# Kernel optimization log

Hardware: AMD Instinct MI355X
Metric: run time of the kernel (lower is better)

## Reference

```python
import jax, jax.numpy as jnp
from jax import lax
import numpy as np

V, D, H, E, L, B = 512, 128, 64, 4, 60, 4096
ADJ = 184  # ((180 + 7) // 8) * 8


def setup_inputs() -> dict:
    key = jax.random.key(0)
    it = iter(jax.random.split(key, 64))

    def nrm(shape, s=0.05):
        return jax.random.normal(next(it), shape, dtype=jnp.float32) * s

    x = jax.random.randint(next(it), (B, L), 0, V, dtype=jnp.int32)
    inp = {"x": x, "emb": nrm((V, D), 0.02).at[0].set(0.0)}  # padding_idx=0 row zero
    for d in ("f", "r"):
        inp[f"w_ih_{d}"] = nrm((4 * H, D)); inp[f"w_hh_{d}"] = nrm((4 * H, H))
        inp[f"b_ih_{d}"] = nrm((4 * H,)); inp[f"b_hh_{d}"] = nrm((4 * H,))
    for p, i_, h_, o_ in (("e", 1, 16, 8), ("l", 1, 16, 8), ("c", V, 32, 16), ("p", 6, 24, 12), ("x", 4, 16, 8)):
        inp[f"{p}_w1"] = nrm((h_, i_)); inp[f"{p}_b1"] = nrm((h_,))
        inp[f"{p}_w2"] = nrm((o_, h_)); inp[f"{p}_b2"] = nrm((o_,))
    inp["fp_w"] = nrm((ADJ, 180)); inp["fp_b"] = nrm((ADJ,))
    inp["attn_w"] = nrm((3 * ADJ, ADJ)); inp["attn_b"] = nrm((3 * ADJ,))
    inp["out_w"] = nrm((ADJ, ADJ)); inp["out_b"] = nrm((ADJ,))
    for i, (o_, i_) in enumerate(((128, ADJ), (64, 128), (32, 64), (E, 32)), 1):
        inp[f"g_w{i}"] = nrm((o_, i_)); inp[f"g_b{i}"] = nrm((o_,))
    return inp


def _mlp2(h, w1, b1, w2, b2):
    return jnp.maximum(h @ w1.T + b1, 0.0) @ w2.T + b2


def _lstm_final(xe, w_ih, w_hh, b_ih, b_hh):
    # torch LSTM gate order i, f, g, o; returns final hidden state [B, H]
    xg = jnp.einsum('bld,gd->blg', xe, w_ih) + b_ih
    h0 = jnp.zeros((xe.shape[0], H), xe.dtype)

    def step(carry, g_t):
        h, c = carry
        g = g_t + h @ w_hh.T + b_hh
        i, f, gg, o = jnp.split(g, 4, axis=-1)
        c = jax.nn.sigmoid(f) * c + jax.nn.sigmoid(i) * jnp.tanh(gg)
        h = jax.nn.sigmoid(o) * jnp.tanh(c)
        return (h, c), None

    (h, _), _ = lax.scan(step, (h0, h0), jnp.swapaxes(xg, 0, 1))
    return h


def _sequence_stats(x):
    # Fully vectorized equivalent of the per-sequence python loops
    f32 = jnp.float32
    mask = x != 0
    vlen = mask.sum(1)                                       # [B]
    vlenf = jnp.maximum(vlen, 1).astype(f32)
    pos = jnp.arange(L)
    # per-row histogram over valid tokens (torch.bincount of valid_seq)
    counts = jnp.zeros((B, V), f32).at[jnp.arange(B)[:, None], x].add(mask.astype(f32))
    probs = counts / jnp.maximum(counts.sum(1, keepdims=True), 1.0)
    entropy = -jnp.sum(probs * jnp.log(probs + 1e-8), axis=1)
    entropy = jnp.where(vlen > 1, entropy, 0.0)
    char_dist = counts / vlenf[:, None]
    # compact valid tokens to the front (torch: seq[seq != 0]), stable argsort
    order = jnp.argsort((~mask).astype(jnp.int32), axis=1)
    cseq = jnp.take_along_axis(x, order, axis=1)
    cseq = jnp.where(pos[None] < vlen[:, None], cseq, 0)
    a, b = cseq[:, :-1], cseq[:, 1:]
    pairmask = pos[: L - 1][None] < (vlen - 1)[:, None]
    den1 = jnp.maximum(vlen - 1, 1).astype(f32)
    repeat = ((a == b) & pairmask).sum(1) / den1
    inc = ((b > a) & pairmask).sum(1) / den1
    dec = ((b < a) & pairmask).sum(1) / den1
    m2 = pos[: L - 2][None] < (vlen - 2)[:, None]
    per = ((cseq[:, :-2] == cseq[:, 2:]) & m2).sum(1) / jnp.maximum(vlen - 2, 1)
    per = jnp.where(vlen >= 4, per, 0.0)
    diversity = (counts > 0).sum(1) / vlenf
    # longest run of equal consecutive tokens via cummax of reset positions
    eq = jnp.concatenate([jnp.zeros((B, 1), bool), (cseq[:, 1:] == cseq[:, :-1]) & (pos[1:][None] < vlen[:, None])], 1)
    lastreset = lax.cummax(jnp.where(eq, -1, pos[None]), axis=1)
    runlen = pos[None] - lastreset + 1
    max_rep = jnp.where(pos[None] < vlen[:, None], runlen, 0).max(1) / vlenf
    pattern = jnp.stack([repeat, inc, dec, per, diversity, max_rep], 1).astype(f32)
    pattern = jnp.where((vlen > 1)[:, None], pattern, 0.0)
    # unique bigrams: sort pair codes, count distinct valid codes
    codes = jnp.where(pairmask, a * V + b, -1)
    s = jnp.sort(codes, axis=1)
    prevc = jnp.concatenate([jnp.full((B, 1), -2, s.dtype), s[:, :-1]], 1)
    comp_ratio = ((s != prevc) & (s >= 0)).sum(1) / den1
    info_density = entropy / jnp.log(jnp.maximum(vlen, 2).astype(f32))
    # local complexity: mean over sliding windows of (#unique / w), w = min(5, len//2)
    wsel = jnp.minimum(5, vlen // 2)
    local = jnp.zeros((B,), f32)
    for w in (2, 3, 4, 5):
        nwin = L - w + 1
        sh = [cseq[:, k:k + nwin] for k in range(w)]
        u = jnp.ones((B, nwin), f32)
        for k in range(1, w):
            isnew = jnp.ones((B, nwin), bool)
            for m in range(k):
                isnew = isnew & (sh[k] != sh[m])
            u = u + isnew
        winmask = pos[:nwin][None] < (vlen - w + 1)[:, None]
        lc = (u * winmask).sum(1) / w / jnp.maximum(vlen - w + 1, 1)
        local = jnp.where(wsel == w, lc, local)
    trans = 1.0 - repeat  # transitions/(len-1) == 1 - repeat_ratio
    complexity = jnp.stack([comp_ratio, info_density, local, trans], 1).astype(f32)
    complexity = jnp.where((vlen > 1)[:, None], complexity, 0.0)
    return entropy, vlen, char_dist, pattern, complexity


def reference(x, emb, w_ih_f, w_hh_f, b_ih_f, b_hh_f, w_ih_r, w_hh_r, b_ih_r, b_hh_r, e_w1, e_b1, e_w2, e_b2, l_w1, l_b1, l_w2, l_b2, c_w1, c_b1, c_w2, c_b2, p_w1, p_b1, p_w2, p_b2, x_w1, x_b1, x_w2, x_b2, fp_w, fp_b, attn_w, attn_b, out_w, out_b, g_w1, g_b1, g_w2, g_b2, g_w3, g_b3, g_w4, g_b4):
    entropy, vlen, char_dist, pattern, complexity = _sequence_stats(x)
    xe = emb[x]                                               # [B, L, D]
    h_f = _lstm_final(xe, w_ih_f, w_hh_f, b_ih_f, b_hh_f)
    h_r = _lstm_final(xe[:, ::-1], w_ih_r, w_hh_r, b_ih_r, b_hh_r)
    feats = jnp.concatenate([
        h_f, h_r,
        _mlp2((entropy / 4.0)[:, None], e_w1, e_b1, e_w2, e_b2),
        _mlp2((vlen.astype(jnp.float32) / 60.0)[:, None], l_w1, l_b1, l_w2, l_b2),
        _mlp2(char_dist, c_w1, c_b1, c_w2, c_b2),
        _mlp2(pattern, p_w1, p_b1, p_w2, p_b2),
        _mlp2(complexity, x_w1, x_b1, x_w2, x_b2),
    ], axis=1)                                                # [B, 180]
    f = feats @ fp_w.T + fp_b                                 # [B, 184]
    # MultiheadAttention with seq_len == 1: softmax over a single key is 1,
    # so attended = out_proj(v_proj(f)) exactly (q/k projections cancel).
    wv, bv = attn_w[2 * ADJ:], attn_b[2 * ADJ:]
    attended = (f @ wv.T + bv) @ out_w.T + out_b
    h = jnp.maximum(attended @ g_w1.T + g_b1, 0.0)
    h = jnp.maximum(h @ g_w2.T + g_b2, 0.0)
    h = jnp.maximum(h @ g_w3.T + g_b3, 0.0)
    logits = h @ g_w4.T + g_b4
    return jax.nn.softmax(logits, axis=-1)  # eval path (training=False)
```

## Files before the change

kernel.cpp:

```cpp
#include <hip/hip_runtime.h>

#define BATCH 4096
#define SEQL  60
#define VOC   512
#define EMBD  128
#define HID   64
#define GATES 256
#define ADJ   184

typedef __attribute__((ext_vector_type(8))) short short8;
typedef __attribute__((ext_vector_type(4))) float f32x4;

__device__ __forceinline__ float sigm(float x) {
  return __builtin_amdgcn_rcpf(1.f + __expf(-x));
}
__device__ __forceinline__ float tanh_(float x) {
  float e = __expf(2.f * x);
  return 1.f - 2.f * __builtin_amdgcn_rcpf(e + 1.f);
}
__device__ __forceinline__ unsigned short f2bf(float f) {
  unsigned int u = __float_as_uint(f);
  unsigned int r = (u + 0x7fffu + ((u >> 16) & 1u)) >> 16;
  return (unsigned short)r;
}
__device__ __forceinline__ float dot4(float4 a, float4 b, float acc) {
  acc = fmaf(a.x, b.x, acc); acc = fmaf(a.y, b.y, acc);
  acc = fmaf(a.z, b.z, acc); acc = fmaf(a.w, b.w, acc);
  return acc;
}
__device__ __forceinline__ float wsumf(float v) {
  #pragma unroll
  for (int s = 32; s > 0; s >>= 1) v += __shfl_xor(v, s, 64);
  return v;
}
__device__ __forceinline__ int wsumi(int v) {
  #pragma unroll
  for (int s = 32; s > 0; s >>= 1) v += __shfl_xor(v, s, 64);
  return v;
}
__device__ __forceinline__ int wmaxi(int v) {
  #pragma unroll
  for (int s = 32; s > 0; s >>= 1) v = max(v, __shfl_xor(v, s, 64));
  return v;
}

__global__ __launch_bounds__(256) void k_mega(
    const int* __restrict__ x, const float* __restrict__ emb,
    const float* __restrict__ wih_f, const float* __restrict__ bif, const float* __restrict__ bhf,
    const float* __restrict__ wih_r, const float* __restrict__ bir, const float* __restrict__ bhr,
    const float* __restrict__ whh_f, const float* __restrict__ whh_r,
    const float* __restrict__ g_w1, const float* __restrict__ g_b1,
    const float* __restrict__ out_w, const float* __restrict__ out_b,
    const float* __restrict__ attn_w, const float* __restrict__ attn_b,
    const float* __restrict__ fp_w, const float* __restrict__ fp_b,
    const float* __restrict__ g_w2, const float* __restrict__ g_w3,
    const float* __restrict__ g_w4, const float* __restrict__ c_w1,
    float* __restrict__ ent_o, float* __restrict__ vlen_o,
    float* __restrict__ pat_o, float* __restrict__ cpx_o,
    unsigned int* __restrict__ cnt_o,
    float* __restrict__ G_f, float* __restrict__ G_r,
    unsigned short* __restrict__ Wfrag,
    float* __restrict__ A, float* __restrict__ avb,
    float* __restrict__ Bp, float* __restrict__ vb,
    float* __restrict__ g_w2t, float* __restrict__ g_w3t, float* __restrict__ g_w4t,
    float* __restrict__ c_w1t) {
  __shared__ unsigned int cnt[4][512];
  __shared__ unsigned short q[4][68];
  const int bid = blockIdx.x;
  const int tid = threadIdx.x;

  if (bid < 1024) {
    const int lane = tid & 63;
    const int wid = tid >> 6;
    const int row = bid * 4 + wid;
    unsigned int* cr = cnt[wid];
    unsigned short* qr = q[wid];

    for (int i = lane; i < 512; i += 64) cr[i] = 0u;
    qr[lane] = 0;
    if (lane < 4) qr[64 + lane] = 0;
    int v = (lane < 60) ? x[row * 60 + lane] : 0;
    bool act = (v != 0);
    unsigned long long amask = __ballot(act);
    int n = __popcll(amask);
    __syncthreads();
    if (act) {
      int pos = __popcll(amask & ((1ull << lane) - 1ull));
      qr[pos] = (unsigned short)v;
      atomicAdd(&cr[v], 1u);
    }
    __syncthreads();

    float vlenf = (float)(n >= 1 ? n : 1);
    float inv = 1.f / vlenf;

    float ent = 0.f; int distinct = 0;
    #pragma unroll
    for (int j = 0; j < 8; j++) {
      unsigned int c = cr[lane + j * 64];
      if (c) {
        distinct++;
        float p = (float)c * inv;
        ent -= p * __logf(p + 1e-8f);
      }
    }
    ent = wsumf(ent);
    distinct = wsumi(distinct);

    int a = qr[lane], b = qr[lane + 1], c2 = qr[lane + 2];
    bool v1 = (lane + 1 < n);
    bool v2 = (lane + 2 < n);
    int rep  = __popcll(__ballot(v1 && (a == b)));
    int incs = __popcll(__ballot(v1 && (b > a)));
    int decs = __popcll(__ballot(v1 && (b < a)));
    int per2 = __popcll(__ballot(v2 && (a == c2)));

    int prev = (lane > 0) ? (int)qr[lane - 1] : -1;
    bool isst = (lane < n) && (lane == 0 || a != prev);
    unsigned long long smask = __ballot(isst);
    int len = 0;
    if (isst) {
      unsigned long long hi = (lane < 63) ? (smask >> (lane + 1)) : 0ull;
      int next = hi ? (lane + __ffsll((unsigned long long)hi)) : n;
      len = next - lane;
    }
    int maxrun = wmaxi(len);

    int code = v1 ? (a * VOC + b) : -1;
    int unique = v1 ? 1 : 0;
    #pragma unroll 1
    for (int j = 0; j < 58; j++) {
      int cj = __shfl(code, j, 64);
      if (j < lane && cj == code) unique = 0;
    }
    int dc = __popcll(__ballot(unique != 0));

    int wl = n >> 1; if (wl > 5) wl = 5;
    float local = 0.f;
    if (wl >= 2) {
      bool pv = (lane + wl <= n);
      int u = 0;
      if (pv) {
        int t0 = qr[lane], t1 = qr[lane + 1], t2 = qr[lane + 2];
        int t3 = qr[lane + 3], t4 = qr[lane + 4];
        u = 1;
        u += (t1 != t0);
        if (wl >= 3) u += (int)((t2 != t1) && (t2 != t0));
        if (wl >= 4) u += (int)((t3 != t2) && (t3 != t1) && (t3 != t0));
        if (wl >= 5) u += (int)((t4 != t3) && (t4 != t2) && (t4 != t1) && (t4 != t0));
      }
      int usum = wsumi(u);
      int denw = n - wl + 1; if (denw < 1) denw = 1;
      local = (float)usum / (float)wl / (float)denw;
    }

    float den1 = (float)((n - 1) >= 1 ? (n - 1) : 1);
    float repeat = (float)rep / den1;
    float per = (n >= 4) ? (float)per2 / (float)((n - 2) >= 1 ? (n - 2) : 1) : 0.f;
    float entz = (n > 1) ? ent : 0.f;
    float z = (n > 1) ? 1.f : 0.f;

    if (lane == 0) {
      ent_o[row] = entz;
      vlen_o[row] = (float)n;
      pat_o[row * 6 + 0] = repeat * z;
      pat_o[row * 6 + 1] = (float)incs / den1 * z;
      pat_o[row * 6 + 2] = (float)decs / den1 * z;
      pat_o[row * 6 + 3] = per * z;
      pat_o[row * 6 + 4] = (float)distinct * inv * z;
      pat_o[row * 6 + 5] = (float)maxrun * inv * z;
      cpx_o[row * 4 + 0] = (float)dc / den1 * z;
      cpx_o[row * 4 + 1] = entz / __logf((float)(n >= 2 ? n : 2)) * z;
      cpx_o[row * 4 + 2] = local * z;
      cpx_o[row * 4 + 3] = (1.f - repeat) * z;
    }
    for (int i = lane; i < 128; i += 64) {
      unsigned int p = cr[4 * i] | (cr[4 * i + 1] << 8) |
                       (cr[4 * i + 2] << 16) | (cr[4 * i + 3] << 24);
      cnt_o[row * 128 + i] = p;
    }
  } else if (bid < 1152) {
    const int bx = bid - 1024;
    const int dir = bx >> 6;
    const int rem = bx & 63;
    const int v0 = (rem >> 2) * 32;
    const int j0 = (rem & 3) * 64;
    const float* W = dir ? wih_r : wih_f;
    const float* bi = dir ? bir : bif;
    const float* bh = dir ? bhr : bhf;
    float* G = dir ? G_r : G_f;
    const int vp = tid >> 4;
    const int jq = tid & 15;
    const int v = v0 + vp * 2;
    const int j = j0 + jq * 4;
    const int gg = j >> 6;
    const int u0 = j & 63;

    const float4* E0 = (const float4*)(emb + (size_t)v * 128);
    const float4* E1 = (const float4*)(emb + (size_t)(v + 1) * 128);
    const float4* W0 = (const float4*)(W + (size_t)j * 128);
    const float4* W1 = (const float4*)(W + (size_t)(j + 1) * 128);
    const float4* W2 = (const float4*)(W + (size_t)(j + 2) * 128);
    const float4* W3 = (const float4*)(W + (size_t)(j + 3) * 128);

    float a00 = 0.f, a01 = 0.f, a02 = 0.f, a03 = 0.f;
    float a10 = 0.f, a11 = 0.f, a12 = 0.f, a13 = 0.f;
    #pragma unroll 4
    for (int d4 = 0; d4 < 32; d4++) {
      float4 e0 = E0[d4], e1 = E1[d4];
      float4 w0 = W0[d4], w1 = W1[d4], w2 = W2[d4], w3 = W3[d4];
      a00 = dot4(e0, w0, a00); a01 = dot4(e0, w1, a01);
      a02 = dot4(e0, w2, a02); a03 = dot4(e0, w3, a03);
      a10 = dot4(e1, w0, a10); a11 = dot4(e1, w1, a11);
      a12 = dot4(e1, w2, a12); a13 = dot4(e1, w3, a13);
    }
    float b0v = bi[j] + bh[j], b1v = bi[j + 1] + bh[j + 1];
    float b2v = bi[j + 2] + bh[j + 2], b3v = bi[j + 3] + bh[j + 3];
    float* g0 = G + (size_t)v * 256 + u0 * 4 + gg;
    g0[0]  = a00 + b0v; g0[4]  = a01 + b1v;
    g0[8]  = a02 + b2v; g0[12] = a03 + b3v;
    float* g1 = g0 + 256;
    g1[0]  = a10 + b0v; g1[4]  = a11 + b1v;
    g1[8]  = a12 + b2v; g1[12] = a13 + b3v;
  } else if (bid < 1280) {
    const int i = bid - 1152;
    const int j = tid;
    const float* g1r = g_w1 + (size_t)i * ADJ;
    if (j < ADJ) {
      float a0 = 0.f, a1 = 0.f, a2 = 0.f, a3 = 0.f;
      for (int k = 0; k < ADJ; k += 4) {
        a0 = fmaf(g1r[k],     out_w[(size_t)(k)     * ADJ + j], a0);
        a1 = fmaf(g1r[k + 1], out_w[(size_t)(k + 1) * ADJ + j], a1);
        a2 = fmaf(g1r[k + 2], out_w[(size_t)(k + 2) * ADJ + j], a2);
        a3 = fmaf(g1r[k + 3], out_w[(size_t)(k + 3) * ADJ + j], a3);
      }
      A[(size_t)i * ADJ + j] = (a0 + a1) + (a2 + a3);
    } else if (j == ADJ) {
      float a0 = 0.f;
      for (int k = 0; k < ADJ; k++) a0 = fmaf(g1r[k], out_b[k], a0);
      avb[i] = a0 + g_b1[i];
    }
  } else if (bid < 1464) {
    const int k = bid - 1280;
    const int j = tid;
    const float* wvr = attn_w + (size_t)(2 * ADJ + k) * ADJ;
    if (j < 180) {
      float a0 = 0.f, a1 = 0.f, a2 = 0.f, a3 = 0.f;
      for (int m = 0; m < ADJ; m += 4) {
        a0 = fmaf(wvr[m],     fp_w[(size_t)(m)     * 180 + j], a0);
        a1 = fmaf(wvr[m + 1], fp_w[(size_t)(m + 1) * 180 + j], a1);
        a2 = fmaf(wvr[m + 2], fp_w[(size_t)(m + 2) * 180 + j], a2);
        a3 = fmaf(wvr[m + 3], fp_w[(size_t)(m + 3) * 180 + j], a3);
      }
      Bp[(size_t)k * 180 + j] = (a0 + a1) + (a2 + a3);
    } else if (j == 180) {
      float a0 = 0.f;
      for (int m = 0; m < ADJ; m++) a0 = fmaf(wvr[m], fp_b[m], a0);
      vb[k] = a0 + attn_b[2 * ADJ + k];
    }
  } else if (bid < 1480) {
    const int id = (bid - 1464) * 256 + tid;
    const int lane = id & 63;
    const int fc = id >> 6;
    const int c = fc & 1;
    const int gg = (fc >> 1) & 3;
    const int w = (fc >> 3) & 3;
    const int dir = fc >> 5;
    const float* whh = dir ? whh_r : whh_f;
    const int n = gg * 64 + w * 16 + (lane & 15);
    const int kb = c * 32 + (lane >> 4) * 8;
    unsigned short* o = Wfrag + (size_t)id * 8;
    #pragma unroll
    for (int j = 0; j < 8; j++) o[j] = f2bf(whh[n * 64 + kb + j]);
  } else if (bid == 1480) {
    for (int i = tid; i < 64 * 128; i += 256) {
      int o = i >> 7, k = i & 127;
      g_w2t[k * 64 + o] = g_w2[i];
    }
    for (int i = tid; i < 32 * 64; i += 256) {
      int o = i >> 6, k = i & 63;
      g_w3t[k * 32 + o] = g_w3[i];
    }
    if (tid < 128) {
      int o = tid >> 5, k = tid & 31;
      g_w4t[k * 4 + o] = g_w4[tid];
    }
  } else {
    const int base = (bid - 1481) * 2048;
    for (int i = tid; i < 2048; i += 256) {
      int idx = base + i;
      int o = idx >> 9, k = idx & 511;
      c_w1t[k * 32 + o] = c_w1[idx];
    }
  }
}

#define LSTM_STEP(T, CUR, NXT)                                                 \
  {                                                                            \
    const unsigned short* hb = hbuf[(T) & 1];                                  \
    short8 a0 = *(const short8*)(hb + ln * 72 + kg * 8);                       \
    short8 a1 = *(const short8*)(hb + ln * 72 + 32 + kg * 8);                  \
    if ((T) < 59) {                                                            \
      int tsn = dir ? (58 - (T)) : ((T) + 1);                                  \
      uint4 of4 = *(const uint4*)(tokoff + tsn * 16 + kg * 4);                 \
      NXT[0] = *(const float4*)(Gb + of4.x + ub);                              \
      NXT[1] = *(const float4*)(Gb + of4.y + ub);                              \
      NXT[2] = *(const float4*)(Gb + of4.z + ub);                              \
      NXT[3] = *(const float4*)(Gb + of4.w + ub);                              \
    }                                                                          \
    f32x4 z0 = {0.f, 0.f, 0.f, 0.f};                                           \
    f32x4 acc0 = z0, acc1 = z0, acc2 = z0, acc3 = z0;                          \
    acc0 = __builtin_amdgcn_mfma_f32_16x16x32_bf16(a0, bfr[0][0], acc0, 0, 0, 0); \
    acc1 = __builtin_amdgcn_mfma_f32_16x16x32_bf16(a0, bfr[1][0], acc1, 0, 0, 0); \
    acc2 = __builtin_amdgcn_mfma_f32_16x16x32_bf16(a0, bfr[2][0], acc2, 0, 0, 0); \
    acc3 = __builtin_amdgcn_mfma_f32_16x16x32_bf16(a0, bfr[3][0], acc3, 0, 0, 0); \
    acc0 = __builtin_amdgcn_mfma_f32_16x16x32_bf16(a1, bfr[0][1], acc0, 0, 0, 0); \
    acc1 = __builtin_amdgcn_mfma_f32_16x16x32_bf16(a1, bfr[1][1], acc1, 0, 0, 0); \
    acc2 = __builtin_amdgcn_mfma_f32_16x16x32_bf16(a1, bfr[2][1], acc2, 0, 0, 0); \
    acc3 = __builtin_amdgcn_mfma_f32_16x16x32_bf16(a1, bfr[3][1], acc3, 0, 0, 0); \
    unsigned short* hw = hbuf[((T) + 1) & 1];                                  \
    _Pragma("unroll")                                                          \
    for (int r = 0; r < 4; r++) {                                              \
      float gi = acc0[r] + CUR[r].x;                                           \
      float gf = acc1[r] + CUR[r].y;                                           \
      float gc = acc2[r] + CUR[r].z;                                           \
      float go = acc3[r] + CUR[r].w;                                           \
      float cn = sigm(gf) * cst[r] + sigm(gi) * tanh_(gc);                     \
      cst[r] = cn;                                                             \
      float h = sigm(go) * tanh_(cn);                                          \
      hw[(kg * 4 + r) * 72 + u] = f2bf(h);                                     \
      if ((T) == 59) ho[(size_t)(b0 + kg * 4 + r) * 64 + u] = h;               \
    }                                                                          \
    __syncthreads();                                                           \
  }

__global__ __launch_bounds__(256) void k_lstm(
    const int* __restrict__ x,
    const float* __restrict__ G_f, const float* __restrict__ G_r,
    const unsigned short* __restrict__ Wfrag,
    const float* __restrict__ A, const float* __restrict__ avb,
    const float* __restrict__ Bp, const float* __restrict__ vb,
    float* __restrict__ C1t, float* __restrict__ c1b,
    float* __restrict__ hf_o, float* __restrict__ hr_o) {
  __shared__ __align__(16) unsigned short hbuf[2][16 * 72];
  __shared__ __align__(16) unsigned int tokoff[60 * 16];
  const int tid = threadIdx.x;

  if (blockIdx.x >= 512) {
    const int i = blockIdx.x - 512, j = tid;
    const float* Ar = A + (size_t)i * ADJ;
    if (j < 180) {
      float a0 = 0.f, a1 = 0.f, a2 = 0.f, a3 = 0.f;
      for (int k = 0; k < ADJ; k += 4) {
        a0 = fmaf(Ar[k],     Bp[(size_t)(k)     * 180 + j], a0);
        a1 = fmaf(Ar[k + 1], Bp[(size_t)(k + 1) * 180 + j], a1);
        a2 = fmaf(Ar[k + 2], Bp[(size_t)(k + 2) * 180 + j], a2);
        a3 = fmaf(Ar[k + 3], Bp[(size_t)(k + 3) * 180 + j], a3);
      }
      C1t[(size_t)j * 128 + i] = (a0 + a1) + (a2 + a3);
    } else if (j == 180) {
      float a0 = 0.f;
      for (int k = 0; k < ADJ; k++) a0 = fmaf(Ar[k], vb[k], a0);
      c1b[i] = a0 + avb[i];
    }
    return;
  }

  const int lane = tid & 63;
  const int w = tid >> 6;
  const int dir = blockIdx.x >> 8;
  const int blk = blockIdx.x & 255;
  const int b0 = blk << 4;
  const float* G = dir ? G_r : G_f;
  const char* Gb = (const char*)G;
  float* ho = dir ? hr_o : hf_o;

  for (int i = tid; i < 960; i += 256) {
    int r = i / 60, t = i - r * 60;
    tokoff[t * 16 + r] = ((unsigned int)x[(size_t)(b0 + r) * 60 + t]) << 10;
  }
  for (int i = tid; i < 16 * 72; i += 256) hbuf[0][i] = 0;

  short8 bfr[4][2];
  #pragma unroll
  for (int gg = 0; gg < 4; gg++)
    #pragma unroll
    for (int c = 0; c < 2; c++) {
      int idx = (((dir * 4 + w) * 4 + gg) * 2 + c) * 64 + lane;
      bfr[gg][c] = *(const short8*)(Wfrag + (size_t)idx * 8);
    }

  const int kg = lane >> 4;
  const int ln = lane & 15;
  const int u = w * 16 + ln;
  const unsigned int ub = (unsigned int)u * 16;
  float cst[4] = {0.f, 0.f, 0.f, 0.f};
  float4 gvA[4], gvB[4];

  __syncthreads();

  {
    int ts0 = dir ? 59 : 0;
    uint4 of4 = *(const uint4*)(tokoff + ts0 * 16 + kg * 4);
    gvA[0] = *(const float4*)(Gb + of4.x + ub);
    gvA[1] = *(const float4*)(Gb + of4.y + ub);
    gvA[2] = *(const float4*)(Gb + of4.z + ub);
    gvA[3] = *(const float4*)(Gb + of4.w + ub);
  }

  #pragma unroll 1
  for (int tt = 0; tt < 30; tt++) {
    const int t0 = tt * 2, t1 = tt * 2 + 1;
    LSTM_STEP(t0, gvA, gvB)
    LSTM_STEP(t1, gvB, gvA)
  }
}

#define FSTR 192
#define CFS  520

__global__ __launch_bounds__(256) void k_head(
    const float* __restrict__ hf, const float* __restrict__ hr,
    const float* __restrict__ ent, const float* __restrict__ vlen,
    const float* __restrict__ pat, const float* __restrict__ cpx,
    const unsigned int* __restrict__ cnts,
    const float* __restrict__ e_w1, const float* __restrict__ e_b1,
    const float* __restrict__ e_w2, const float* __restrict__ e_b2,
    const float* __restrict__ l_w1, const float* __restrict__ l_b1,
    const float* __restrict__ l_w2, const float* __restrict__ l_b2,
    const float* __restrict__ c_w1t, const float* __restrict__ c_b1,
    const float* __restrict__ c_w2, const float* __restrict__ c_b2,
    const float* __restrict__ p_w1, const float* __restrict__ p_b1,
    const float* __restrict__ p_w2, const float* __restrict__ p_b2,
    const float* __restrict__ x_w1, const float* __restrict__ x_b1,
    const float* __restrict__ x_w2, const float* __restrict__ x_b2,
    const float* __restrict__ C1t, const float* __restrict__ c1b,
    const float* __restrict__ g_w2t, const float* __restrict__ g_b2,
    const float* __restrict__ g_w3t, const float* __restrict__ g_b3,
    const float* __restrict__ g_w4t, const float* __restrict__ g_b4,
    float* __restrict__ out) {
  __shared__ float feat[8 * FSTR];
  __shared__ float cf[8 * CFS];
  __shared__ float h1[8 * 128];
  __shared__ float h2[8 * 64];
  __shared__ float h3[8 * 32];
  __shared__ float h1c[8 * 33];
  __shared__ float lg[32];
  const int tid = threadIdx.x;
  const int b0 = blockIdx.x * 8;

  if (tid < 128) {
    int r = tid >> 4, c = tid & 15;
    float4 vv = ((const float4*)(hf + (size_t)(b0 + r) * 64))[c];
    *(float4*)(feat + r * FSTR + c * 4) = vv;
  } else {
    int t = tid - 128;
    int r = t >> 4, c = t & 15;
    float4 vv = ((const float4*)(hr + (size_t)(b0 + r) * 64))[c];
    *(float4*)(feat + r * FSTR + 64 + c * 4) = vv;
  }
  {
    uint4 u4v = *(const uint4*)(cnts + (size_t)b0 * 128 + tid * 4);
    int r = tid >> 5, c0 = (tid & 31) * 16;
    float* dst = cf + r * CFS + c0;
    unsigned int uu[4] = {u4v.x, u4v.y, u4v.z, u4v.w};
    #pragma unroll
    for (int qq = 0; qq < 4; qq++) {
      float4 f4;
      f4.x = (float)(uu[qq] & 255u);
      f4.y = (float)((uu[qq] >> 8) & 255u);
      f4.z = (float)((uu[qq] >> 16) & 255u);
      f4.w = (float)(uu[qq] >> 24);
      *(float4*)(dst + qq * 4) = f4;
    }
  }
  __syncthreads();
  {
    int o = tid & 31, r = tid >> 5;
    const float* cv = cf + r * CFS;
    float a0 = 0.f, a1 = 0.f, a2 = 0.f, a3 = 0.f;
    #pragma unroll 4
    for (int k = 0; k < 512; k += 4) {
      float4 c4 = *(const float4*)(cv + k);
      a0 = fmaf(c_w1t[(k + 0) * 32 + o], c4.x, a0);
      a1 = fmaf(c_w1t[(k + 1) * 32 + o], c4.y, a1);
      a2 = fmaf(c_w1t[(k + 2) * 32 + o], c4.z, a2);
      a3 = fmaf(c_w1t[(k + 3) * 32 + o], c4.w, a3);
    }
    float invv = __builtin_amdgcn_rcpf(fmaxf(vlen[b0 + r], 1.f));
    h1c[r * 33 + o] = fmaxf(((a0 + a1) + (a2 + a3)) * invv + c_b1[o], 0.f);
  }
  __syncthreads();
  if (tid < 32) {
    const int m = tid & 3, r = tid >> 2, b = b0 + r;
    float tt[24];
    if (m == 0) {
      float ein = ent[b] * 0.25f;
      #pragma unroll
      for (int o = 0; o < 16; o++) tt[o] = fmaxf(e_w1[o] * ein + e_b1[o], 0.f);
      #pragma unroll
      for (int o = 0; o < 8; o++) {
        float a = e_b2[o];
        #pragma unroll
        for (int k = 0; k < 16; k++) a = fmaf(e_w2[o * 16 + k], tt[k], a);
        feat[r * FSTR + 128 + o] = a;
      }
    } else if (m == 1) {
      float lin = vlen[b] * (1.f / 60.f);
      #pragma unroll
      for (int o = 0; o < 16; o++) tt[o] = fmaxf(l_w1[o] * lin + l_b1[o], 0.f);
      #pragma unroll
      for (int o = 0; o < 8; o++) {
        float a = l_b2[o];
        #pragma unroll
        for (int k = 0; k < 16; k++) a = fmaf(l_w2[o * 16 + k], tt[k], a);
        feat[r * FSTR + 136 + o] = a;
      }
    } else if (m == 2) {
      float pin[6];
      #pragma unroll
      for (int k = 0; k < 6; k++) pin[k] = pat[b * 6 + k];
      #pragma unroll
      for (int o = 0; o < 24; o++) {
        float a = p_b1[o];
        #pragma unroll
        for (int k = 0; k < 6; k++) a = fmaf(p_w1[o * 6 + k], pin[k], a);
        tt[o] = fmaxf(a, 0.f);
      }
      #pragma unroll
      for (int o = 0; o < 12; o++) {
        float a = p_b2[o];
        #pragma unroll
        for (int k = 0; k < 24; k++) a = fmaf(p_w2[o * 24 + k], tt[k], a);
        feat[r * FSTR + 160 + o] = a;
      }
    } else {
      float xin[4];
      #pragma unroll
      for (int k = 0; k < 4; k++) xin[k] = cpx[b * 4 + k];
      #pragma unroll
      for (int o = 0; o < 16; o++) {
        float a = x_b1[o];
        #pragma unroll
        for (int k = 0; k < 4; k++) a = fmaf(x_w1[o * 4 + k], xin[k], a);
        tt[o] = fmaxf(a, 0.f);
      }
      #pragma unroll
      for (int o = 0; o < 8; o++) {
        float a = x_b2[o];
        #pragma unroll
        for (int k = 0; k < 16; k++) a = fmaf(x_w2[o * 16 + k], tt[k], a);
        feat[r * FSTR + 172 + o] = a;
      }
    }
  } else if (tid >= 64 && tid < 192) {
    int t = tid - 64;
    int r = t >> 4, o = t & 15;
    float a = c_b2[o];
    const float* hh = h1c + r * 33;
    #pragma unroll
    for (int k = 0; k < 32; k++) a = fmaf(c_w2[o * 32 + k], hh[k], a);
    feat[r * FSTR + 144 + o] = a;
  }
  __syncthreads();

  {
    const int o = tid & 127, rg = tid >> 7;
    const float* f0p = feat + (rg * 4 + 0) * FSTR;
    const float* f1p = feat + (rg * 4 + 1) * FSTR;
    const float* f2p = feat + (rg * 4 + 2) * FSTR;
// ... 46 lines not shown
    float bb = g_b2[o];
    h2[(rg * 2 + 0) * 64 + o] = fmaxf(a0 + bb, 0.f);
    h2[(rg * 2 + 1) * 64 + o] = fmaxf(a1 + bb, 0.f);
  }
  __syncthreads();
  {
    const int o = tid & 31, rg = tid >> 5;
    const float* fp = h2 + rg * 64;
    float a = 0.f;
    #pragma unroll 4
    for (int k4 = 0; k4 < 16; k4++) {
      float w0 = g_w3t[(k4 * 4 + 0) * 32 + o];
      float w1 = g_w3t[(k4 * 4 + 1) * 32 + o];
      float w2 = g_w3t[(k4 * 4 + 2) * 32 + o];
      float w3 = g_w3t[(k4 * 4 + 3) * 32 + o];
      float4 f0 = *(const float4*)(fp + k4 * 4);
      a = fmaf(w0, f0.x, a); a = fmaf(w1, f0.y, a);
      a = fmaf(w2, f0.z, a); a = fmaf(w3, f0.w, a);
    }
    h3[rg * 32 + o] = fmaxf(a + g_b3[o], 0.f);
  }
  __syncthreads();
  if (tid < 32) {
    int r = tid >> 2, o = tid & 3;
    const float* hh = h3 + r * 32;
    float a = g_b4[o];
    #pragma unroll
    for (int k = 0; k < 32; k++) a = fmaf(g_w4t[k * 4 + o], hh[k], a);
    lg[tid] = a;
  }
  __syncthreads();
  if (tid < 8) {
    float l0 = lg[tid * 4 + 0], l1 = lg[tid * 4 + 1];
    float l2 = lg[tid * 4 + 2], l3 = lg[tid * 4 + 3];
    float m = fmaxf(fmaxf(l0, l1), fmaxf(l2, l3));
    float e0 = __expf(l0 - m), e1 = __expf(l1 - m);
    float e2 = __expf(l2 - m), e3 = __expf(l3 - m);
    float is = __builtin_amdgcn_rcpf(e0 + e1 + e2 + e3);
    float4 o4; o4.x = e0 * is; o4.y = e1 * is; o4.z = e2 * is; o4.w = e3 * is;
    *(float4*)(out + (size_t)(b0 + tid) * 4) = o4;
  }
}

extern "C" void kernel_launch(void* const* d_in, const int* in_sizes, int n_in,
                              void* d_out, int out_size, void* d_ws, size_t ws_size,
                              hipStream_t stream) {
  const int*   x     = (const int*)d_in[0];
  const float* emb   = (const float*)d_in[1];
  const float* wih_f = (const float*)d_in[2];
  const float* whh_f = (const float*)d_in[3];
  const float* bih_f = (const float*)d_in[4];
  const float* bhh_f = (const float*)d_in[5];
  const float* wih_r = (const float*)d_in[6];
  const float* whh_r = (const float*)d_in[7];
  const float* bih_r = (const float*)d_in[8];
  const float* bhh_r = (const float*)d_in[9];
  const float* e_w1 = (const float*)d_in[10]; const float* e_b1 = (const float*)d_in[11];
  const float* e_w2 = (const float*)d_in[12]; const float* e_b2 = (const float*)d_in[13];
  const float* l_w1 = (const float*)d_in[14]; const float* l_b1 = (const float*)d_in[15];
  const float* l_w2 = (const float*)d_in[16]; const float* l_b2 = (const float*)d_in[17];
  const float* c_w1 = (const float*)d_in[18]; const float* c_b1 = (const float*)d_in[19];
  const float* c_w2 = (const float*)d_in[20]; const float* c_b2 = (const float*)d_in[21];
  const float* p_w1 = (const float*)d_in[22]; const float* p_b1 = (const float*)d_in[23];
  const float* p_w2 = (const float*)d_in[24]; const float* p_b2 = (const float*)d_in[25];
  const float* x_w1 = (const float*)d_in[26]; const float* x_b1 = (const float*)d_in[27];
  const float* x_w2 = (const float*)d_in[28]; const float* x_b2 = (const float*)d_in[29];
  const float* fp_w = (const float*)d_in[30]; const float* fp_b = (const float*)d_in[31];
  const float* attn_w = (const float*)d_in[32]; const float* attn_b = (const float*)d_in[33];
  const float* out_w = (const float*)d_in[34]; const float* out_b = (const float*)d_in[35];
  const float* g_w1 = (const float*)d_in[36]; const float* g_b1 = (const float*)d_in[37];
  const float* g_w2 = (const float*)d_in[38]; const float* g_b2 = (const float*)d_in[39];
  const float* g_w3 = (const float*)d_in[40]; const float* g_b3 = (const float*)d_in[41];
  const float* g_w4 = (const float*)d_in[42]; const float* g_b4 = (const float*)d_in[43];

  float* ws   = (float*)d_ws;
  float* G_f  = ws;
  float* G_r  = G_f  + 512 * 256;
  float* hfw  = G_r  + 512 * 256;
  float* hrw  = hfw  + BATCH * 64;
  float* entw = hrw  + BATCH * 64;
  float* vlnw = entw + BATCH;
  float* patw = vlnw + BATCH;
  float* cpxw = patw + BATCH * 6;
  unsigned int* cntw = (unsigned int*)(cpxw + BATCH * 4);
  float* Aw   = (float*)(cntw + BATCH * 128);
  float* avbw = Aw + 128 * ADJ;
  float* Bpw  = avbw + 128;
  float* vbw  = Bpw + ADJ * 180;
  float* C1t  = vbw + ADJ;
  float* c1b  = C1t + 180 * 128;
  float* g2t  = c1b + 128;
  float* g3t  = g2t + 128 * 64;
  float* g4t  = g3t + 64 * 32;
  float* cw1t = g4t + 32 * 4;
  unsigned short* Wfrag = (unsigned short*)(cw1t + 512 * 32);

  k_mega<<<dim3(1489), dim3(256), 0, stream>>>(
      x, emb, wih_f, bih_f, bhh_f, wih_r, bih_r, bhh_r, whh_f, whh_r,
      g_w1, g_b1, out_w, out_b, attn_w, attn_b, fp_w, fp_b,
      g_w2, g_w3, g_w4, c_w1,
      entw, vlnw, patw, cpxw, cntw, G_f, G_r, Wfrag,
      Aw, avbw, Bpw, vbw, g2t, g3t, g4t, cw1t);
  k_lstm<<<dim3(640), dim3(256), 0, stream>>>(
      x, G_f, G_r, Wfrag, Aw, avbw, Bpw, vbw, C1t, c1b, hfw, hrw);
  k_head<<<dim3(BATCH / 8), dim3(256), 0, stream>>>(
      hfw, hrw, entw, vlnw, patw, cpxw, cntw,
      e_w1, e_b1, e_w2, e_b2, l_w1, l_b1, l_w2, l_b2,
      cw1t, c_b1, c_w2, c_b2, p_w1, p_b1, p_w2, p_b2,
      x_w1, x_b1, x_w2, x_b2, C1t, c1b,
      g2t, g_b2, g3t, g_b3, g4t, g_b4,
      (float*)d_out);
}
```

Baseline: 260.4 us.

## Move per-row stats into LSTM kernel and compute char MLP via token gather

Per-row sequence statistics move from the weight-prep kernel into the LSTM launch, so they run on idle CUs alongside the 512 LSTM blocks instead of ahead of them. The packed 512-bin histogram workspace is dropped: the char-distribution first layer now sums transposed c_w1 rows gathered by token id, with the padding row zeroed, in place of a 512-long dot product over counts. A cheaper non-RNE bf16 conversion helper is also added, though Wfrag packing still uses the RNE version. Extra shared memory in the combined kernel may lower LSTM occupancy.

After: 247.3 us. 1.05x faster.

```diff
diff --git a/kernel.cpp b/kernel.cpp
--- a/kernel.cpp
+++ b/kernel.cpp
@@ -18,10 +18,13 @@
   float e = __expf(2.f * x);
   return 1.f - 2.f * __builtin_amdgcn_rcpf(e + 1.f);
 }
-__device__ __forceinline__ unsigned short f2bf(float f) {
+__device__ __forceinline__ unsigned short f2bf_rne(float f) {
   unsigned int u = __float_as_uint(f);
   unsigned int r = (u + 0x7fffu + ((u >> 16) & 1u)) >> 16;
   return (unsigned short)r;
+}
+__device__ __forceinline__ unsigned short f2bf(float f) {
+  return (unsigned short)((__float_as_uint(f) + 0x8000u) >> 16);
 }
 __device__ __forceinline__ float dot4(float4 a, float4 b, float acc) {
   acc = fmaf(a.x, b.x, acc); acc = fmaf(a.y, b.y, acc);
@@ -44,8 +47,8 @@
   return v;
 }
 
-__global__ __launch_bounds__(256) void k_mega(
-    const int* __restrict__ x, const float* __restrict__ emb,
+__global__ __launch_bounds__(256) void k_prep(
+    const float* __restrict__ emb,
     const float* __restrict__ wih_f, const float* __restrict__ bif, const float* __restrict__ bhf,
     const float* __restrict__ wih_r, const float* __restrict__ bir, const float* __restrict__ bhr,
     const float* __restrict__ whh_f, const float* __restrict__ whh_r,
@@ -55,134 +58,18 @@
     const float* __restrict__ fp_w, const float* __restrict__ fp_b,
     const float* __restrict__ g_w2, const float* __restrict__ g_w3,
     const float* __restrict__ g_w4, const float* __restrict__ c_w1,
-    float* __restrict__ ent_o, float* __restrict__ vlen_o,
-    float* __restrict__ pat_o, float* __restrict__ cpx_o,
-    unsigned int* __restrict__ cnt_o,
     float* __restrict__ G_f, float* __restrict__ G_r,
     unsigned short* __restrict__ Wfrag,
     float* __restrict__ A, float* __restrict__ avb,
     float* __restrict__ Bp, float* __restrict__ vb,
     float* __restrict__ g_w2t, float* __restrict__ g_w3t, float* __restrict__ g_w4t,
     float* __restrict__ c_w1t) {
-  __shared__ unsigned int cnt[4][512];
-  __shared__ unsigned short q[4][68];
   const int bid = blockIdx.x;
   const int tid = threadIdx.x;
 
-  if (bid < 1024) {
-    const int lane = tid & 63;
-    const int wid = tid >> 6;
-    const int row = bid * 4 + wid;
-    unsigned int* cr = cnt[wid];
-    unsigned short* qr = q[wid];
-
-    for (int i = lane; i < 512; i += 64) cr[i] = 0u;
-    qr[lane] = 0;
-    if (lane < 4) qr[64 + lane] = 0;
-    int v = (lane < 60) ? x[row * 60 + lane] : 0;
-    bool act = (v != 0);
-    unsigned long long amask = __ballot(act);
-    int n = __popcll(amask);
-    __syncthreads();
-    if (act) {
-      int pos = __popcll(amask & ((1ull << lane) - 1ull));
-      qr[pos] = (unsigned short)v;
-      atomicAdd(&cr[v], 1u);
-    }
-    __syncthreads();
-
-    float vlenf = (float)(n >= 1 ? n : 1);
-    float inv = 1.f / vlenf;
-
-    float ent = 0.f; int distinct = 0;
-    #pragma unroll
-    for (int j = 0; j < 8; j++) {
-      unsigned int c = cr[lane + j * 64];
-      if (c) {
-        distinct++;
-        float p = (float)c * inv;
-        ent -= p * __logf(p + 1e-8f);
-      }
-    }
-    ent = wsumf(ent);
-    distinct = wsumi(distinct);
-
-    int a = qr[lane], b = qr[lane + 1], c2 = qr[lane + 2];
-    bool v1 = (lane + 1 < n);
-    bool v2 = (lane + 2 < n);
-    int rep  = __popcll(__ballot(v1 && (a == b)));
-    int incs = __popcll(__ballot(v1 && (b > a)));
-    int decs = __popcll(__ballot(v1 && (b < a)));
-    int per2 = __popcll(__ballot(v2 && (a == c2)));
-
-    int prev = (lane > 0) ? (int)qr[lane - 1] : -1;
-    bool isst = (lane < n) && (lane == 0 || a != prev);
-    unsigned long long smask = __ballot(isst);
-    int len = 0;
-    if (isst) {
-      unsigned long long hi = (lane < 63) ? (smask >> (lane + 1)) : 0ull;
-      int next = hi ? (lane + __ffsll((unsigned long long)hi)) : n;
-      len = next - lane;
-    }
-    int maxrun = wmaxi(len);
-
-    int code = v1 ? (a * VOC + b) : -1;
-    int unique = v1 ? 1 : 0;
-    #pragma unroll 1
-    for (int j = 0; j < 58; j++) {
-      int cj = __shfl(code, j, 64);
-      if (j < lane && cj == code) unique = 0;
-    }
-    int dc = __popcll(__ballot(unique != 0));
-
-    int wl = n >> 1; if (wl > 5) wl = 5;
-    float local = 0.f;
-    if (wl >= 2) {
-      bool pv = (lane + wl <= n);
-      int u = 0;
-      if (pv) {
-        int t0 = qr[lane], t1 = qr[lane + 1], t2 = qr[lane + 2];
-        int t3 = qr[lane + 3], t4 = qr[lane + 4];
-        u = 1;
-        u += (t1 != t0);
-        if (wl >= 3) u += (int)((t2 != t1) && (t2 != t0));
-        if (wl >= 4) u += (int)((t3 != t2) && (t3 != t1) && (t3 != t0));
-        if (wl >= 5) u += (int)((t4 != t3) && (t4 != t2) && (t4 != t1) && (t4 != t0));
-      }
-      int usum = wsumi(u);
-      int denw = n - wl + 1; if (denw < 1) denw = 1;
-      local = (float)usum / (float)wl / (float)denw;
-    }
-
-    float den1 = (float)((n - 1) >= 1 ? (n - 1) : 1);
-    float repeat = (float)rep / den1;
-    float per = (n >= 4) ? (float)per2 / (float)((n - 2) >= 1 ? (n - 2) : 1) : 0.f;
-    float entz = (n > 1) ? ent : 0.f;
-    float z = (n > 1) ? 1.f : 0.f;
-
-    if (lane == 0) {
-      ent_o[row] = entz;
-      vlen_o[row] = (float)n;
-      pat_o[row * 6 + 0] = repeat * z;
-      pat_o[row * 6 + 1] = (float)incs / den1 * z;
-      pat_o[row * 6 + 2] = (float)decs / den1 * z;
-      pat_o[row * 6 + 3] = per * z;
-      pat_o[row * 6 + 4] = (float)distinct * inv * z;
-      pat_o[row * 6 + 5] = (float)maxrun * inv * z;
-      cpx_o[row * 4 + 0] = (float)dc / den1 * z;
-      cpx_o[row * 4 + 1] = entz / __logf((float)(n >= 2 ? n : 2)) * z;
-      cpx_o[row * 4 + 2] = local * z;
-      cpx_o[row * 4 + 3] = (1.f - repeat) * z;
-    }
-    for (int i = lane; i < 128; i += 64) {
-      unsigned int p = cr[4 * i] | (cr[4 * i + 1] << 8) |
-                       (cr[4 * i + 2] << 16) | (cr[4 * i + 3] << 24);
-      cnt_o[row * 128 + i] = p;
-    }
-  } else if (bid < 1152) {
-    const int bx = bid - 1024;
-    const int dir = bx >> 6;
-    const int rem = bx & 63;
+  if (bid < 128) {
+    const int dir = bid >> 6;
+    const int rem = bid & 63;
     const int v0 = (rem >> 2) * 32;
     const int j0 = (rem & 3) * 64;
     const float* W = dir ? wih_r : wih_f;
@@ -222,44 +109,8 @@
     float* g1 = g0 + 256;
     g1[0]  = a10 + b0v; g1[4]  = a11 + b1v;
     g1[8]  = a12 + b2v; g1[12] = a13 + b3v;
-  } else if (bid < 1280) {
-    const int i = bid - 1152;
-    const int j = tid;
-    const float* g1r = g_w1 + (size_t)i * ADJ;
-    if (j < ADJ) {
-      float a0 = 0.f, a1 = 0.f, a2 = 0.f, a3 = 0.f;
-      for (int k = 0; k < ADJ; k += 4) {
-        a0 = fmaf(g1r[k],     out_w[(size_t)(k)     * ADJ + j], a0);
-        a1 = fmaf(g1r[k + 1], out_w[(size_t)(k + 1) * ADJ + j], a1);
-        a2 = fmaf(g1r[k + 2], out_w[(size_t)(k + 2) * ADJ + j], a2);
-        a3 = fmaf(g1r[k + 3], out_w[(size_t)(k + 3) * ADJ + j], a3);
-      }
-      A[(size_t)i * ADJ + j] = (a0 + a1) + (a2 + a3);
-    } else if (j == ADJ) {
-      float a0 = 0.f;
-      for (int k = 0; k < ADJ; k++) a0 = fmaf(g1r[k], out_b[k], a0);
-      avb[i] = a0 + g_b1[i];
-    }
-  } else if (bid < 1464) {
-    const int k = bid - 1280;
-    const int j = tid;
-    const float* wvr = attn_w + (size_t)(2 * ADJ + k) * ADJ;
-    if (j < 180) {
-      float a0 = 0.f, a1 = 0.f, a2 = 0.f, a3 = 0.f;
-      for (int m = 0; m < ADJ; m += 4) {
-        a0 = fmaf(wvr[m],     fp_w[(size_t)(m)     * 180 + j], a0);
-        a1 = fmaf(wvr[m + 1], fp_w[(size_t)(m + 1) * 180 + j], a1);
-        a2 = fmaf(wvr[m + 2], fp_w[(size_t)(m + 2) * 180 + j], a2);
-        a3 = fmaf(wvr[m + 3], fp_w[(size_t)(m + 3) * 180 + j], a3);
-      }
-      Bp[(size_t)k * 180 + j] = (a0 + a1) + (a2 + a3);
-    } else if (j == 180) {
-      float a0 = 0.f;
-      for (int m = 0; m < ADJ; m++) a0 = fmaf(wvr[m], fp_b[m], a0);
-      vb[k] = a0 + attn_b[2 * ADJ + k];
-    }
-  } else if (bid < 1480) {
-    const int id = (bid - 1464) * 256 + tid;
+  } else if (bid < 144) {
+    const int id = (bid - 128) * 256 + tid;
     const int lane = id & 63;
     const int fc = id >> 6;
     const int c = fc & 1;
@@ -271,8 +122,44 @@
     const int kb = c * 32 + (lane >> 4) * 8;
     unsigned short* o = Wfrag + (size_t)id * 8;
     #pragma unroll
-    for (int j = 0; j < 8; j++) o[j] = f2bf(whh[n * 64 + kb + j]);
-  } else if (bid == 1480) {
+    for (int j = 0; j < 8; j++) o[j] = f2bf_rne(whh[n * 64 + kb + j]);
+  } else if (bid < 272) {
+    const int i = bid - 144;
+    const int j = tid;
+    const float* g1r = g_w1 + (size_t)i * ADJ;
+    if (j < ADJ) {
+      float a0 = 0.f, a1 = 0.f, a2 = 0.f, a3 = 0.f;
+      for (int k = 0; k < ADJ; k += 4) {
+        a0 = fmaf(g1r[k],     out_w[(size_t)(k)     * ADJ + j], a0);
+        a1 = fmaf(g1r[k + 1], out_w[(size_t)(k + 1) * ADJ + j], a1);
+        a2 = fmaf(g1r[k + 2], out_w[(size_t)(k + 2) * ADJ + j], a2);
+        a3 = fmaf(g1r[k + 3], out_w[(size_t)(k + 3) * ADJ + j], a3);
+      }
+      A[(size_t)i * ADJ + j] = (a0 + a1) + (a2 + a3);
+    } else if (j == ADJ) {
+      float a0 = 0.f;
+      for (int k = 0; k < ADJ; k++) a0 = fmaf(g1r[k], out_b[k], a0);
+      avb[i] = a0 + g_b1[i];
+    }
+  } else if (bid < 456) {
+    const int k = bid - 272;
+    const int j = tid;
+    const float* wvr = attn_w + (size_t)(2 * ADJ + k) * ADJ;
+    if (j < 180) {
+      float a0 = 0.f, a1 = 0.f, a2 = 0.f, a3 = 0.f;
+      for (int m = 0; m < ADJ; m += 4) {
+        a0 = fmaf(wvr[m],     fp_w[(size_t)(m)     * 180 + j], a0);
+        a1 = fmaf(wvr[m + 1], fp_w[(size_t)(m + 1) * 180 + j], a1);
+        a2 = fmaf(wvr[m + 2], fp_w[(size_t)(m + 2) * 180 + j], a2);
+        a3 = fmaf(wvr[m + 3], fp_w[(size_t)(m + 3) * 180 + j], a3);
+      }
+      Bp[(size_t)k * 180 + j] = (a0 + a1) + (a2 + a3);
+    } else if (j == 180) {
+      float a0 = 0.f;
+      for (int m = 0; m < ADJ; m++) a0 = fmaf(wvr[m], fp_b[m], a0);
+      vb[k] = a0 + attn_b[2 * ADJ + k];
+    }
+  } else if (bid == 456) {
     for (int i = tid; i < 64 * 128; i += 256) {
       int o = i >> 7, k = i & 127;
       g_w2t[k * 64 + o] = g_w2[i];
@@ -286,11 +173,11 @@
       g_w4t[k * 4 + o] = g_w4[tid];
     }
   } else {
-    const int base = (bid - 1481) * 2048;
+    const int base = (bid - 457) * 2048;
     for (int i = tid; i < 2048; i += 256) {
       int idx = base + i;
       int o = idx >> 9, k = idx & 511;
-      c_w1t[k * 32 + o] = c_w1[idx];
+      c_w1t[k * 32 + o] = k ? c_w1[o * 512 + k] : 0.f;
     }
   }
 }
@@ -334,20 +221,179 @@
     __syncthreads();                                                           \
   }
 
-__global__ __launch_bounds__(256) void k_lstm(
+__global__ __launch_bounds__(256) void k_main(
     const int* __restrict__ x,
     const float* __restrict__ G_f, const float* __restrict__ G_r,
     const unsigned short* __restrict__ Wfrag,
     const float* __restrict__ A, const float* __restrict__ avb,
     const float* __restrict__ Bp, const float* __restrict__ vb,
     float* __restrict__ C1t, float* __restrict__ c1b,
-    float* __restrict__ hf_o, float* __restrict__ hr_o) {
+    float* __restrict__ hf_o, float* __restrict__ hr_o,
+    float* __restrict__ ent_o, float* __restrict__ vlen_o,
+    float* __restrict__ pat_o, float* __restrict__ cpx_o) {
   __shared__ __align__(16) unsigned short hbuf[2][16 * 72];
   __shared__ __align__(16) unsigned int tokoff[60 * 16];
+  __shared__ unsigned int cnt[4][512];
+  __shared__ unsigned short q[4][68];
+  const int bid = blockIdx.x;
   const int tid = threadIdx.x;
 
-  if (blockIdx.x >= 512) {
-    const int i = blockIdx.x - 512, j = tid;
+  if (bid < 512) {
+    const int lane = tid & 63;
+    const int w = tid >> 6;
+    const int dir = bid >> 8;
+    const int blk = bid & 255;
+    const int b0 = blk << 4;
+    const float* G = dir ? G_r : G_f;
+    const char* Gb = (const char*)G;
+    float* ho = dir ? hr_o : hf_o;
+
+    for (int i = tid; i < 960; i += 256) {
+      int r = i / 60, t = i - r * 60;
+      tokoff[t * 16 + r] = ((unsigned int)x[(size_t)(b0 + r) * 60 + t]) << 10;
+    }
+    for (int i = tid; i < 16 * 72; i += 256) hbuf[0][i] = 0;
+
+    short8 bfr[4][2];
+    #pragma unroll
+    for (int gg = 0; gg < 4; gg++)
+      #pragma unroll
+      for (int c = 0; c < 2; c++) {
+        int idx = (((dir * 4 + w) * 4 + gg) * 2 + c) * 64 + lane;
+        bfr[gg][c] = *(const short8*)(Wfrag + (size_t)idx * 8);
+      }
+
+    const int kg = lane >> 4;
+    const int ln = lane & 15;
+    const int u = w * 16 + ln;
+    const unsigned int ub = (unsigned int)u * 16;
+    float cst[4] = {0.f, 0.f, 0.f, 0.f};
+    float4 gvA[4], gvB[4];
+
+    __syncthreads();
+
+    {
+      int ts0 = dir ? 59 : 0;
+      uint4 of4 = *(const uint4*)(tokoff + ts0 * 16 + kg * 4);
+      gvA[0] = *(const float4*)(Gb + of4.x + ub);
+      gvA[1] = *(const float4*)(Gb + of4.y + ub);
+      gvA[2] = *(const float4*)(Gb + of4.z + ub);
+      gvA[3] = *(const float4*)(Gb + of4.w + ub);
+    }
+
+    #pragma unroll 1
+    for (int tt = 0; tt < 30; tt++) {
+      const int t0 = tt * 2, t1 = tt * 2 + 1;
+      LSTM_STEP(t0, gvA, gvB)
+      LSTM_STEP(t1, gvB, gvA)
+    }
+  } else if (bid < 1536) {
+    const int lane = tid & 63;
+    const int wid = tid >> 6;
+    const int row = (bid - 512) * 4 + wid;
+    unsigned int* cr = cnt[wid];
+    unsigned short* qr = q[wid];
+
+    for (int i = lane; i < 512; i += 64) cr[i] = 0u;
+    qr[lane] = 0;
+    if (lane < 4) qr[64 + lane] = 0;
+    int v = (lane < 60) ? x[row * 60 + lane] : 0;
+    bool act = (v != 0);
+    unsigned long long amask = __ballot(act);
+    int n = __popcll(amask);
+    __syncthreads();
+    if (act) {
+      int pos = __popcll(amask & ((1ull << lane) - 1ull));
+      qr[pos] = (unsigned short)v;
+      atomicAdd(&cr[v], 1u);
+    }
+    __syncthreads();
+
+    float vlenf = (float)(n >= 1 ? n : 1);
+    float inv = 1.f / vlenf;
+
+    float ent = 0.f; int distinct = 0;
+    #pragma unroll
+    for (int j = 0; j < 8; j++) {
+      unsigned int c = cr[lane + j * 64];
+      if (c) {
+        distinct++;
+        float p = (float)c * inv;
+        ent -= p * __logf(p + 1e-8f);
+      }
+    }
+    ent = wsumf(ent);
+    distinct = wsumi(distinct);
+
+    int a = qr[lane], b = qr[lane + 1], c2 = qr[lane + 2];
+    bool v1 = (lane + 1 < n);
+    bool v2 = (lane + 2 < n);
+    int rep  = __popcll(__ballot(v1 && (a == b)));
+    int incs = __popcll(__ballot(v1 && (b > a)));
+    int decs = __popcll(__ballot(v1 && (b < a)));
+    int per2 = __popcll(__ballot(v2 && (a == c2)));
+
+    int prev = (lane > 0) ? (int)qr[lane - 1] : -1;
+    bool isst = (lane < n) && (lane == 0 || a != prev);
+    unsigned long long smask = __ballot(isst);
+    int len = 0;
+    if (isst) {
+      unsigned long long hi = (lane < 63) ? (smask >> (lane + 1)) : 0ull;
+      int next = hi ? (lane + __ffsll((unsigned long long)hi)) : n;
+      len = next - lane;
+    }
+    int maxrun = wmaxi(len);
+
+    int code = v1 ? (a * VOC + b) : -1;
+    int unique = v1 ? 1 : 0;
+    #pragma unroll 1
+    for (int j = 0; j < 58; j++) {
+      int cj = __shfl(code, j, 64);
+      if (j < lane && cj == code) unique = 0;
+    }
+    int dc = __popcll(__ballot(unique != 0));
+
+    int wl = n >> 1; if (wl > 5) wl = 5;
+    float local = 0.f;
+    if (wl >= 2) {
+      bool pv = (lane + wl <= n);
+      int u = 0;
+      if (pv) {
+        int t0 = qr[lane], t1 = qr[lane + 1], t2 = qr[lane + 2];
+        int t3 = qr[lane + 3], t4 = qr[lane + 4];
+        u = 1;
+        u += (t1 != t0);
+        if (wl >= 3) u += (int)((t2 != t1) && (t2 != t0));
+        if (wl >= 4) u += (int)((t3 != t2) && (t3 != t1) && (t3 != t0));
+        if (wl >= 5) u += (int)((t4 != t3) && (t4 != t2) && (t4 != t1) && (t4 != t0));
+      }
+      int usum = wsumi(u);
+      int denw = n - wl + 1; if (denw < 1) denw = 1;
+      local = (float)usum / (float)wl / (float)denw;
+    }
+
+    float den1 = (float)((n - 1) >= 1 ? (n - 1) : 1);
+    float repeat = (float)rep / den1;
+    float per = (n >= 4) ? (float)per2 / (float)((n - 2) >= 1 ? (n - 2) : 1) : 0.f;
+    float entz = (n > 1) ? ent : 0.f;
+    float z = (n > 1) ? 1.f : 0.f;
+
+    if (lane == 0) {
+      ent_o[row] = entz;
+      vlen_o[row] = (float)n;
+      pat_o[row * 6 + 0] = repeat * z;
+      pat_o[row * 6 + 1] = (float)incs / den1 * z;
+      pat_o[row * 6 + 2] = (float)decs / den1 * z;
+      pat_o[row * 6 + 3] = per * z;
+      pat_o[row * 6 + 4] = (float)distinct * inv * z;
+      pat_o[row * 6 + 5] = (float)maxrun * inv * z;
+      cpx_o[row * 4 + 0] = (float)dc / den1 * z;
+      cpx_o[row * 4 + 1] = entz / __logf((float)(n >= 2 ? n : 2)) * z;
+      cpx_o[row * 4 + 2] = local * z;
+      cpx_o[row * 4 + 3] = (1.f - repeat) * z;
+    }
+  } else {
+    const int i = bid - 1536, j = tid;
     const float* Ar = A + (size_t)i * ADJ;
     if (j < 180) {
       float a0 = 0.f, a1 = 0.f, a2 = 0.f, a3 = 0.f;
@@ -363,67 +409,16 @@
       for (int k = 0; k < ADJ; k++) a0 = fmaf(Ar[k], vb[k], a0);
       c1b[i] = a0 + avb[i];
     }
-    return;
-  }
-
-  const int lane = tid & 63;
-  const int w = tid >> 6;
-  const int dir = blockIdx.x >> 8;
-  const int blk = blockIdx.x & 255;
-  const int b0 = blk << 4;
-  const float* G = dir ? G_r : G_f;
-  const char* Gb = (const char*)G;
-  float* ho = dir ? hr_o : hf_o;
-
-  for (int i = tid; i < 960; i += 256) {
-    int r = i / 60, t = i - r * 60;
-    tokoff[t * 16 + r] = ((unsigned int)x[(size_t)(b0 + r) * 60 + t]) << 10;
-  }
-  for (int i = tid; i < 16 * 72; i += 256) hbuf[0][i] = 0;
-
-  short8 bfr[4][2];
-  #pragma unroll
-  for (int gg = 0; gg < 4; gg++)
-    #pragma unroll
-    for (int c = 0; c < 2; c++) {
-      int idx = (((dir * 4 + w) * 4 + gg) * 2 + c) * 64 + lane;
-      bfr[gg][c] = *(const short8*)(Wfrag + (size_t)idx * 8);
-    }
-
-  const int kg = lane >> 4;
-  const int ln = lane & 15;
-  const int u = w * 16 + ln;
-  const unsigned int ub = (unsigned int)u * 16;
-  float cst[4] = {0.f, 0.f, 0.f, 0.f};
-  float4 gvA[4], gvB[4];
-
-  __syncthreads();
-
-  {
-    int ts0 = dir ? 59 : 0;
-    uint4 of4 = *(const uint4*)(tokoff + ts0 * 16 + kg * 4);
-    gvA[0] = *(const float4*)(Gb + of4.x + ub);
-    gvA[1] = *(const float4*)(Gb + of4.y + ub);
-    gvA[2] = *(const float4*)(Gb + of4.z + ub);
-    gvA[3] = *(const float4*)(Gb + of4.w + ub);
-  }
-
-  #pragma unroll 1
-  for (int tt = 0; tt < 30; tt++) {
-    const int t0 = tt * 2, t1 = tt * 2 + 1;
-    LSTM_STEP(t0, gvA, gvB)
-    LSTM_STEP(t1, gvB, gvA)
   }
 }
 
 #define FSTR 192
-#define CFS  520
 
 __global__ __launch_bounds__(256) void k_head(
+    const int* __restrict__ x,
     const float* __restrict__ hf, const float* __restrict__ hr,
     const float* __restrict__ ent, const float* __restrict__ vlen,
     const float* __restrict__ pat, const float* __restrict__ cpx,
-    const unsigned int* __restrict__ cnts,
     const float* __restrict__ e_w1, const float* __restrict__ e_b1,
     const float* __restrict__ e_w2, const float* __restrict__ e_b2,
     const float* __restrict__ l_w1, const float* __restrict__ l_b1,
@@ -440,7 +435,7 @@
     const float* __restrict__ g_w4t, const float* __restrict__ g_b4,
     float* __restrict__ out) {
   __shared__ float feat[8 * FSTR];
-  __shared__ float cf[8 * CFS];
+  __shared__ unsigned short tk[8 * 64];
   __shared__ float h1[8 * 128];
   __shared__ float h2[8 * 64];
   __shared__ float h3[8 * 32];
@@ -459,33 +454,22 @@
     float4 vv = ((const float4*)(hr + (size_t)(b0 + r) * 64))[c];
     *(float4*)(feat + r * FSTR + 64 + c * 4) = vv;
   }
-  {
-    uint4 u4v = *(const uint4*)(cnts + (size_t)b0 * 128 + tid * 4);
-    int r = tid >> 5, c0 = (tid & 31) * 16;
-    float* dst = cf + r * CFS + c0;
-    unsigned int uu[4] = {u4v.x, u4v.y, u4v.z, u4v.w};
-    #pragma unroll
-    for (int qq = 0; qq < 4; qq++) {
-      float4 f4;
-      f4.x = (float)(uu[qq] & 255u);
-      f4.y = (float)((uu[qq] >> 8) & 255u);
-      f4.z = (float)((uu[qq] >> 16) & 255u);
-      f4.w = (float)(uu[qq] >> 24);
-      *(float4*)(dst + qq * 4) = f4;
-    }
+  for (int i = tid; i < 480; i += 256) {
+    int r = i / 60, t = i - r * 60;
+    tk[r * 64 + t] = (unsigned short)x[(size_t)(b0 + r) * 60 + t];
   }
   __syncthreads();
   {
     int o = tid & 31, r = tid >> 5;
-    const float* cv = cf + r * CFS;
+    const unsigned short* tkr = tk + r * 64;
     float a0 = 0.f, a1 = 0.f, a2 = 0.f, a3 = 0.f;
-    #pragma unroll 4
-    for (int k = 0; k < 512; k += 4) {
-      float4 c4 = *(const float4*)(cv + k);
-      a0 = fmaf(c_w1t[(k + 0) * 32 + o], c4.x, a0);
-      a1 = fmaf(c_w1t[(k + 1) * 32 + o], c4.y, a1);
-      a2 = fmaf(c_w1t[(k + 2) * 32 + o], c4.z, a2);
-      a3 = fmaf(c_w1t[(k + 3) * 32 + o], c4.w, a3);
+    #pragma unroll 5
+    for (int t = 0; t < 60; t += 4) {
+      int t0 = tkr[t], t1 = tkr[t + 1], t2 = tkr[t + 2], t3 = tkr[t + 3];
+      a0 += c_w1t[t0 * 32 + o];
+      a1 += c_w1t[t1 * 32 + o];
+      a2 += c_w1t[t2 * 32 + o];
+      a3 += c_w1t[t3 * 32 + o];
     }
     float invv = __builtin_amdgcn_rcpf(fmaxf(vlen[b0 + r], 1.f));
     h1c[r * 33 + o] = fmaxf(((a0 + a1) + (a2 + a3)) * invv + c_b1[o], 0.f);
@@ -698,8 +682,7 @@
   float* vlnw = entw + BATCH;
   float* patw = vlnw + BATCH;
   float* cpxw = patw + BATCH * 6;
-  unsigned int* cntw = (unsigned int*)(cpxw + BATCH * 4);
-  float* Aw   = (float*)(cntw + BATCH * 128);
+  float* Aw   = cpxw + BATCH * 4;
   float* avbw = Aw + 128 * ADJ;
   float* Bpw  = avbw + 128;
   float* vbw  = Bpw + ADJ * 180;
@@ -711,16 +694,16 @@
   float* cw1t = g4t + 32 * 4;
   unsigned short* Wfrag = (unsigned short*)(cw1t + 512 * 32);
 
-  k_mega<<<dim3(1489), dim3(256), 0, stream>>>(
-      x, emb, wih_f, bih_f, bhh_f, wih_r, bih_r, bhh_r, whh_f, whh_r,
+  k_prep<<<dim3(465), dim3(256), 0, stream>>>(
+      emb, wih_f, bih_f, bhh_f, wih_r, bih_r, bhh_r, whh_f, whh_r,
       g_w1, g_b1, out_w, out_b, attn_w, attn_b, fp_w, fp_b,
       g_w2, g_w3, g_w4, c_w1,
-      entw, vlnw, patw, cpxw, cntw, G_f, G_r, Wfrag,
-      Aw, avbw, Bpw, vbw, g2t, g3t, g4t, cw1t);
-  k_lstm<<<dim3(640), dim3(256), 0, stream>>>(
-      x, G_f, G_r, Wfrag, Aw, avbw, Bpw, vbw, C1t, c1b, hfw, hrw);
+      G_f, G_r, Wfrag, Aw, avbw, Bpw, vbw, g2t, g3t, g4t, cw1t);
+  k_main<<<dim3(1664), dim3(256), 0, stream>>>(
+      x, G_f, G_r, Wfrag, Aw, avbw, Bpw, vbw, C1t, c1b,
+      hfw, hrw, entw, vlnw, patw, cpxw);
   k_head<<<dim3(BATCH / 8), dim3(256), 0, stream>>>(
-      hfw, hrw, entw, vlnw, patw, cpxw, cntw,
+      x, hfw, hrw, entw, vlnw, patw, cpxw,
       e_w1, e_b1, e_w2, e_b2, l_w1, l_b1, l_w2, l_b2,
       cw1t, c_b1, c_w2, c_b2, p_w1, p_b1, p_w2, p_b2,
       x_w1, x_b1, x_w2, x_b2, C1t, c1b,
```
